# Kernel optimization log

Hardware: AMD Instinct MI355X
Metric: run time of the kernel (lower is better)

## Reference

```python
import jax, jax.numpy as jnp
import numpy as np

# torchvision Grayscale luminance weights
_GRAY_W = np.array([0.2989, 0.587, 0.114], dtype=np.float32)

# Unnormalized DCT-II matrix as used by torch_dct.dct(norm=None):
#   X_k = 2 * sum_n x_n * cos(pi * (2n+1) * k / (2N)),  N = 8
_N = 8
_n = np.arange(_N)
_DCT_M = (2.0 * np.cos(np.pi * (2.0 * _n[None, :] + 1.0) * _n[:, None] / (2.0 * _N))).astype(np.float32)  # [k, n]


def setup_inputs() -> dict:
    key = jax.random.key(0)
    # (B, C, T, H, W) video batch in [0, 1)
    x = jax.random.uniform(key, (8, 3, 32, 256, 256), dtype=jnp.float32)
    return {"x": x}


def reference(x):
    B, C, T, H, W = x.shape
    # permute (B, C, T, H, W) -> (B, T, C, H, W)
    x = jnp.transpose(x, (0, 2, 1, 3, 4))
    # Grayscale: weighted sum over channel dim, then squeeze -> (B, T, H, W)
    gw = jnp.asarray(_GRAY_W, dtype=x.dtype)
    g = jnp.einsum('btchw,c->bthw', x, gw)
    # unfold(2,8,8).unfold(3,8,8) -> (B, T, H/8, W/8, 8, 8) non-overlapping blocks
    hb, wb = H // _N, W // _N
    blocks = g.reshape(B, T, hb, _N, wb, _N)
    blocks = jnp.transpose(blocks, (0, 1, 2, 4, 3, 5))  # (B, T, hb, wb, 8, 8)
    blocks = blocks.reshape(B, T, hb * wb, _N, _N)
    # dct_2d(norm=None): DCT-II along last dim, then along second-to-last
    # == D @ X @ D^T for each 8x8 block
    D = jnp.asarray(_DCT_M, dtype=x.dtype)
    out = jnp.einsum('kn,btpnm,lm->btpkl', D, blocks, D)
    return out
```

## Files before the change

### kernel.cpp

```cpp
#include <hip/hip_runtime.h>


#define TPB 256

__global__ __launch_bounds__(TPB) void dct_gray_kernel(
    const float* __restrict__ x, float* __restrict__ out) {
  constexpr int T = 32, H = 256, W = 256;
  __shared__ float g[8][256];
  __shared__ float Dm[64];

  const int wg  = blockIdx.x;
  const int tid = threadIdx.x;
  const int bt  = wg >> 5;
  const int hb  = wg & 31;

  if (tid < 64) {
    const int k = tid >> 3, n = tid & 7;
    Dm[tid] = 2.0f * cosf(0.19634954084936207f * (float)((2 * n + 1) * k));
  }

  const int b = bt >> 5;
  const int t = bt & 31;
  const size_t cstride = (size_t)T * H * W;
  const size_t base0 =
      ((size_t)(b * 3) * T + (size_t)t) * (size_t)(H * W) + (size_t)hb * 8 * W;

  const float w0 = 0.2989f, w1 = 0.587f, w2 = 0.114f;

#pragma unroll
  for (int i = tid; i < 512; i += TPB) {
    const int r  = i >> 6;
    const int c4 = i & 63;
    const size_t off = base0 + (size_t)r * W + (size_t)(c4 * 4);
    const float4 a = *(const float4*)(x + off);
    const float4 bb = *(const float4*)(x + off + cstride);
    const float4 cc = *(const float4*)(x + off + 2 * cstride);
    float4 gg;
    gg.x = w0 * a.x + w1 * bb.x + w2 * cc.x;
    gg.y = w0 * a.y + w1 * bb.y + w2 * cc.y;
    gg.z = w0 * a.z + w1 * bb.z + w2 * cc.z;
    gg.w = w0 * a.w + w1 * bb.w + w2 * cc.w;
    *(float4*)(&g[r][c4 * 4]) = gg;
  }
  __syncthreads();

  const int p = tid >> 3;
  const int k = tid & 7;

  float temp[8];
#pragma unroll
  for (int m = 0; m < 8; ++m) temp[m] = 0.0f;
#pragma unroll
  for (int n = 0; n < 8; ++n) {
    const float dkn = Dm[k * 8 + n];
    const float4 g0 = *(const float4*)(&g[n][p * 8]);
    const float4 g1 = *(const float4*)(&g[n][p * 8 + 4]);
    temp[0] += dkn * g0.x; temp[1] += dkn * g0.y;
    temp[2] += dkn * g0.z; temp[3] += dkn * g0.w;
    temp[4] += dkn * g1.x; temp[5] += dkn * g1.y;
    temp[6] += dkn * g1.z; temp[7] += dkn * g1.w;
  }

  float res[8];
#pragma unroll
  for (int l = 0; l < 8; ++l) {
    float acc = 0.0f;
#pragma unroll
    for (int m = 0; m < 8; ++m) acc += temp[m] * Dm[l * 8 + m];
    res[l] = acc;
  }

  float* o = out + (size_t)wg * 2048 + (size_t)tid * 8;
  *(float4*)(o)     = make_float4(res[0], res[1], res[2], res[3]);
  *(float4*)(o + 4) = make_float4(res[4], res[5], res[6], res[7]);
}

extern "C" void kernel_launch(void* const* d_in, const int* in_sizes, int n_in,
                              void* d_out, int out_size, void* d_ws, size_t ws_size,
                              hipStream_t stream) {
  const float* x = (const float*)d_in[0];
  float* out = (float*)d_out;
  dct_gray_kernel<<<8192, TPB, 0, stream>>>(x, out);
}
```

Before: 289.4 us.

## Make DCT kernel persistent with double-buffered prefetch and nontemporal memory ops

```diff
diff --git a/kernel.cpp b/kernel.cpp
--- a/kernel.cpp
+++ b/kernel.cpp
@@ -2,83 +2,125 @@
 
 
 #define TPB 256
+typedef float f4 __attribute__((ext_vector_type(4)));
 
 __global__ __launch_bounds__(TPB) void dct_gray_kernel(
     const float* __restrict__ x, float* __restrict__ out) {
   constexpr int T = 32, H = 256, W = 256;
-  __shared__ float g[8][256];
+  constexpr int NSTRIPS = 8192;
+  constexpr int GRID = 2048;
+  constexpr int ITERS = NSTRIPS / GRID;
+
+  __shared__ float g[2][8][256];
   __shared__ float Dm[64];
 
-  const int wg  = blockIdx.x;
   const int tid = threadIdx.x;
-  const int bt  = wg >> 5;
-  const int hb  = wg & 31;
 
   if (tid < 64) {
-    const int k = tid >> 3, n = tid & 7;
-    Dm[tid] = 2.0f * cosf(0.19634954084936207f * (float)((2 * n + 1) * k));
+    const int kk = tid >> 3, nn = tid & 7;
+    Dm[tid] = 2.0f * cosf(0.19634954084936207f * (float)((2 * nn + 1) * kk));
   }
 
-  const int b = bt >> 5;
-  const int t = bt & 31;
+  const float w0 = 0.2989f, w1 = 0.587f, w2 = 0.114f;
   const size_t cstride = (size_t)T * H * W;
-  const size_t base0 =
-      ((size_t)(b * 3) * T + (size_t)t) * (size_t)(H * W) + (size_t)hb * 8 * W;
-
-  const float w0 = 0.2989f, w1 = 0.587f, w2 = 0.114f;
-
-#pragma unroll
-  for (int i = tid; i < 512; i += TPB) {
-    const int r  = i >> 6;
-    const int c4 = i & 63;
-    const size_t off = base0 + (size_t)r * W + (size_t)(c4 * 4);
-    const float4 a = *(const float4*)(x + off);
-    const float4 bb = *(const float4*)(x + off + cstride);
-    const float4 cc = *(const float4*)(x + off + 2 * cstride);
-    float4 gg;
-    gg.x = w0 * a.x + w1 * bb.x + w2 * cc.x;
-    gg.y = w0 * a.y + w1 * bb.y + w2 * cc.y;
-    gg.z = w0 * a.z + w1 * bb.z + w2 * cc.z;
-    gg.w = w0 * a.w + w1 * bb.w + w2 * cc.w;
-    *(float4*)(&g[r][c4 * 4]) = gg;
-  }
-  __syncthreads();
 
   const int p = tid >> 3;
   const int k = tid & 7;
 
-  float temp[8];
+  float dk[8];
 #pragma unroll
-  for (int m = 0; m < 8; ++m) temp[m] = 0.0f;
+  for (int n = 0; n < 8; ++n)
+    dk[n] = 2.0f * cosf(0.19634954084936207f * (float)((2 * n + 1) * k));
+
+  auto strip_base = [&](int sidx) -> size_t {
+    const int bt = sidx >> 5;
+    const int hb = sidx & 31;
+    const int b = bt >> 5;
+    const int t = bt & 31;
+    return ((size_t)(b * 3) * T + (size_t)t) * (size_t)(H * W) +
+           (size_t)hb * 8 * W;
+  };
+
+  {
+    const size_t base0 = strip_base(blockIdx.x);
+    f4 A[2], B[2], C[2];
 #pragma unroll
-  for (int n = 0; n < 8; ++n) {
-    const float dkn = Dm[k * 8 + n];
-    const float4 g0 = *(const float4*)(&g[n][p * 8]);
-    const float4 g1 = *(const float4*)(&g[n][p * 8 + 4]);
-    temp[0] += dkn * g0.x; temp[1] += dkn * g0.y;
-    temp[2] += dkn * g0.z; temp[3] += dkn * g0.w;
-    temp[4] += dkn * g1.x; temp[5] += dkn * g1.y;
-    temp[6] += dkn * g1.z; temp[7] += dkn * g1.w;
+    for (int j = 0; j < 2; ++j) {
+      const int i = tid + j * TPB;
+      const size_t off =
+          base0 + (size_t)(i >> 6) * W + (size_t)((i & 63) * 4);
+      A[j] = __builtin_nontemporal_load((const f4*)(x + off));
+      B[j] = __builtin_nontemporal_load((const f4*)(x + off + cstride));
+      C[j] = __builtin_nontemporal_load((const f4*)(x + off + 2 * cstride));
+    }
+#pragma unroll
+    for (int j = 0; j < 2; ++j) {
+      const int i = tid + j * TPB;
+      f4 gg = w0 * A[j] + w1 * B[j] + w2 * C[j];
+      *(f4*)(&g[0][i >> 6][(i & 63) * 4]) = gg;
+    }
   }
+  __syncthreads();
 
-  float res[8];
+  for (int s = 0; s < ITERS; ++s) {
+    const int cur = s & 1;
+    const int sidx = blockIdx.x + s * GRID;
+
+    f4 A[2], B[2], C[2];
+    const bool more = (s + 1 < ITERS);
+    if (more) {
+      const size_t basep = strip_base(blockIdx.x + (s + 1) * GRID);
 #pragma unroll
-  for (int l = 0; l < 8; ++l) {
-    float acc = 0.0f;
+      for (int j = 0; j < 2; ++j) {
+        const int i = tid + j * TPB;
+        const size_t off =
+            basep + (size_t)(i >> 6) * W + (size_t)((i & 63) * 4);
+        A[j] = __builtin_nontemporal_load((const f4*)(x + off));
+        B[j] = __builtin_nontemporal_load((const f4*)(x + off + cstride));
+        C[j] = __builtin_nontemporal_load((const f4*)(x + off + 2 * cstride));
+      }
+    }
+
+    f4 t0 = {0.f, 0.f, 0.f, 0.f}, t1 = {0.f, 0.f, 0.f, 0.f};
 #pragma unroll
-    for (int m = 0; m < 8; ++m) acc += temp[m] * Dm[l * 8 + m];
-    res[l] = acc;
+    for (int n = 0; n < 8; ++n) {
+      const float dkn = dk[n];
+      const f4 g0 = *(const f4*)(&g[cur][n][p * 8]);
+      const f4 g1 = *(const f4*)(&g[cur][n][p * 8 + 4]);
+      t0 += dkn * g0;
+      t1 += dkn * g1;
+    }
+    float res[8];
+#pragma unroll
+    for (int l = 0; l < 8; ++l) {
+      const f4 d0 = *(const f4*)(&Dm[l * 8]);
+      const f4 d1 = *(const f4*)(&Dm[l * 8 + 4]);
+      res[l] = t0.x * d0.x + t0.y * d0.y + t0.z * d0.z + t0.w * d0.w +
+               t1.x * d1.x + t1.y * d1.y + t1.z * d1.z + t1.w * d1.w;
+    }
+
+    float* o = out + (size_t)sidx * 2048 + (size_t)tid * 8;
+    f4 v0 = {res[0], res[1], res[2], res[3]};
+    f4 v1 = {res[4], res[5], res[6], res[7]};
+    __builtin_nontemporal_store(v0, (f4*)o);
+    __builtin_nontemporal_store(v1, (f4*)(o + 4));
+
+    if (more) {
+#pragma unroll
+      for (int j = 0; j < 2; ++j) {
+        const int i = tid + j * TPB;
+        f4 gg = w0 * A[j] + w1 * B[j] + w2 * C[j];
+        *(f4*)(&g[cur ^ 1][i >> 6][(i & 63) * 4]) = gg;
+      }
+    }
+    __syncthreads();
   }
-
-  float* o = out + (size_t)wg * 2048 + (size_t)tid * 8;
-  *(float4*)(o)     = make_float4(res[0], res[1], res[2], res[3]);
-  *(float4*)(o + 4) = make_float4(res[4], res[5], res[6], res[7]);
 }
 
 extern "C" void kernel_launch(void* const* d_in, const int* in_sizes, int n_in,
-                              void* d_out, int out_size, void* d_ws, size_t ws_size,
-                              hipStream_t stream) {
+                              void* d_out, int out_size, void* d_ws,
+                              size_t ws_size, hipStream_t stream) {
   const float* x = (const float*)d_in[0];
   float* out = (float*)d_out;
-  dct_gray_kernel<<<8192, TPB, 0, stream>>>(x, out);
+  dct_gray_kernel<<<2048, TPB, 0, stream>>>(x, out);
 }
```

After: 288.8 us. Within noise of the previous version (-0.2%).
